# Kernel tuning notes

Hardware: AMD Instinct MI355X
Metric: run time of the kernel (lower is better)

## Reference

```python
import jax, jax.numpy as jnp
import numpy as np

D_MODEL, D_STATE, D_CONV, EXPAND = 768, 16, 4, 2
D_INNER = EXPAND * D_MODEL
DT_RANK = -(-D_MODEL // 16)  # ceil(d_model/16) = 48
LN_EPS = 1e-5


def setup_inputs() -> dict:
    key = jax.random.key(0)
    ks = jax.random.split(key, 12)
    B, L = 8, 1024
    s = 0.02
    x = jax.random.normal(ks[0], (B, L, D_MODEL), jnp.float32)
    ln_g = jnp.ones((D_MODEL,), jnp.float32)
    ln_b = jnp.zeros((D_MODEL,), jnp.float32)
    W_in = jax.random.normal(ks[1], (D_MODEL, 2 * D_INNER), jnp.float32) * s
    conv_w = jax.random.normal(ks[2], (D_INNER, 1, D_CONV), jnp.float32) * s
    conv_b = jnp.zeros((D_INNER,), jnp.float32)
    W_x = jax.random.normal(ks[3], (D_INNER, DT_RANK + 2 * D_STATE), jnp.float32) * s
    W_dt = jax.random.normal(ks[4], (DT_RANK, D_INNER), jnp.float32) * s
    b_dt = jax.random.uniform(ks[5], (D_INNER,), jnp.float32, -4.0, -2.0)  # softplus -> small dt
    # S4D-real init: A_log[d, n] = log(n+1)
    A_log = jnp.log(jnp.tile(jnp.arange(1, D_STATE + 1, dtype=jnp.float32), (D_INNER, 1)))
    Dskip = jnp.ones((D_INNER,), jnp.float32)
    W_out = jax.random.normal(ks[6], (D_INNER, D_MODEL), jnp.float32) * s
    return dict(x=x, ln_g=ln_g, ln_b=ln_b, W_in=W_in, conv_w=conv_w, conv_b=conv_b,
                W_x=W_x, W_dt=W_dt, b_dt=b_dt, A_log=A_log, Dskip=Dskip, W_out=W_out)


def _mamba_mixer(x, ln_g, ln_b, W_in, conv_w, conv_b, W_x, W_dt, b_dt, A_log, Dskip, W_out):
    B, L, _ = x.shape
    d_inner, _, d_conv = conv_w.shape
    d_state = A_log.shape[1]

    # LayerNorm
    mu = x.mean(-1, keepdims=True)
    var = ((x - mu) ** 2).mean(-1, keepdims=True)
    xn = (x - mu) * jax.lax.rsqrt(var + LN_EPS) * ln_g + ln_b

    # Input projection -> (x_part, z gate)
    xz = xn @ W_in                      # (B, L, 2*d_inner)
    xp, z = jnp.split(xz, 2, axis=-1)

    # Causal depthwise conv1d over time
    xc = jax.lax.conv_general_dilated(
        xp.transpose(0, 2, 1), conv_w,
        window_strides=(1,), padding=[(d_conv - 1, 0)],
        dimension_numbers=("NCH", "OIH", "NCH"), feature_group_count=d_inner)
    xc = jax.nn.silu(xc + conv_b[None, :, None]).transpose(0, 2, 1)  # (B, L, d_inner)

    # Selective parameters
    x_dbl = xc @ W_x                    # (B, L, dt_rank + 2*d_state)
    dt, Bm, Cm = jnp.split(x_dbl, [DT_RANK, DT_RANK + d_state], axis=-1)
    dt = jax.nn.softplus(dt @ W_dt + b_dt)   # (B, L, d_inner)
    A = -jnp.exp(A_log)                      # (d_inner, d_state)

    # Selective (S6) scan over time, carrying state h: (B, d_inner, d_state)
    def step(h, inp):
        x_t, dt_t, B_t, C_t = inp            # (B,d_in), (B,d_in), (B,d_state), (B,d_state)
        dA = jnp.exp(dt_t[:, :, None] * A)   # (B, d_inner, d_state)
        h = dA * h + dt_t[:, :, None] * B_t[:, None, :] * x_t[:, :, None]
        y = jnp.einsum('bds,bs->bd', h, C_t)
        return h, y

    h0 = jnp.zeros((B, d_inner, d_state), x.dtype)
    xs = (xc.transpose(1, 0, 2), dt.transpose(1, 0, 2),
          Bm.transpose(1, 0, 2), Cm.transpose(1, 0, 2))
    _, ys = jax.lax.scan(step, h0, xs)       # ys: (L, B, d_inner)
    y = ys.transpose(1, 0, 2) + xc * Dskip

    # Gate, output projection, residual (dropout is identity in eval mode)
    y = y * jax.nn.silu(z)
    return y @ W_out + x


def reference(x, ln_g, ln_b, W_in, conv_w, conv_b, W_x, W_dt, b_dt, A_log, Dskip, W_out):
    return _mamba_mixer(x, ln_g, ln_b, W_in, conv_w, conv_b, W_x, W_dt, b_dt, A_log, Dskip, W_out)
```

## Files before the change

### kernel.cpp

```cpp
#include <hip/hip_runtime.h>

typedef unsigned short u16;
typedef unsigned int u32;
typedef u16 u16x4 __attribute__((ext_vector_type(4)));
typedef u16 u16x8 __attribute__((ext_vector_type(8)));
typedef __bf16 bf16x8 __attribute__((ext_vector_type(8)));
typedef float f32x4 __attribute__((ext_vector_type(4)));

#define DEV static __device__ __forceinline__
#define AS1 __attribute__((address_space(1)))
#define AS3 __attribute__((address_space(3)))

DEV float bf2f(u16 u) {
  union { u32 i; float f; } c; c.i = ((u32)u) << 16; return c.f;
}
DEV u16 f2bf(float f) {
  union { float f; u32 i; } c; c.f = f;
  u32 x = c.i;
  return (u16)((x + 0x7fffu + ((x >> 16) & 1u)) >> 16);
}

DEV void pow_tree(float e1, float* f) {
  f[1] = e1;        f[2] = e1 * e1;   f[3] = f[1] * f[2]; f[4] = f[2] * f[2];
  f[5] = f[1] * f[4]; f[6] = f[2] * f[4]; f[7] = f[3] * f[4]; f[8] = f[4] * f[4];
  f[9] = f[1] * f[8]; f[10] = f[2] * f[8]; f[11] = f[3] * f[8]; f[12] = f[4] * f[8];
  f[13] = f[5] * f[8]; f[14] = f[6] * f[8]; f[15] = f[7] * f[8]; f[16] = f[8] * f[8];
}

__global__ __launch_bounds__(256) void k_ln(const float* __restrict__ x, const float* __restrict__ g,
                                            const float* __restrict__ b, u16* __restrict__ xn) {
  int row = blockIdx.x, t = threadIdx.x;
  const float* xr = x + (size_t)row * 768;
  float v0 = xr[t], v1 = xr[t + 256], v2 = xr[t + 512];
  float s = v0 + v1 + v2, s2 = v0 * v0 + v1 * v1 + v2 * v2;
#pragma unroll
  for (int o = 32; o; o >>= 1) { s += __shfl_xor(s, o, 64); s2 += __shfl_xor(s2, o, 64); }
  __shared__ float ps[4], ps2[4];
  int wv = t >> 6;
  if ((t & 63) == 0) { ps[wv] = s; ps2[wv] = s2; }
  __syncthreads();
  s = ps[0] + ps[1] + ps[2] + ps[3];
  s2 = ps2[0] + ps2[1] + ps2[2] + ps2[3];
  float mu = s * (1.f / 768.f);
  float var = s2 * (1.f / 768.f) - mu * mu;
  float rs = rsqrtf(var + 1e-5f);
  u16* o = xn + (size_t)row * 768;
  o[t]       = f2bf((v0 - mu) * rs * g[t]       + b[t]);
  o[t + 256] = f2bf((v1 - mu) * rs * g[t + 256] + b[t + 256]);
  o[t + 512] = f2bf((v2 - mu) * rs * g[t + 512] + b[t + 512]);
}

__global__ __launch_bounds__(256) void k_prep(const float* __restrict__ Win, const float* __restrict__ Wout,
                                              const float* __restrict__ Wx,
                                              u16* __restrict__ Wt_in, u16* __restrict__ Wt_out,
                                              u16* __restrict__ Wxt) {
  int bid = blockIdx.x, tid = threadIdx.x;
  if (bid < 3456) {
    const float* in; u16* out; int R, C, bx, by;
    if (bid < 2304) { in = Win;  out = Wt_in;  R = 768;  C = 3072; bx = bid % 96; by = bid / 96; }
    else { int b2 = bid - 2304; in = Wout; out = Wt_out; R = 1536; C = 768;  bx = b2 % 24; by = b2 / 24; }
    __shared__ u16 tile[32][33];
    int tx = tid & 31, ty = tid >> 5;
    int x = bx * 32 + tx, y0 = by * 32;
#pragma unroll
    for (int j = 0; j < 32; j += 8)
      tile[ty + j][tx] = f2bf(in[(size_t)(y0 + ty + j) * C + x]);
    __syncthreads();
    int ox = y0 + tx, oy0 = bx * 32;
#pragma unroll
    for (int j = 0; j < 32; j += 8)
      out[(size_t)(oy0 + ty + j) * R + ox] = tile[tx][ty + j];
  } else {
    int idx = (bid - 3456) * 256 + tid;
    int c = idx / 1536, r = idx % 1536;
    Wxt[idx] = (c < 80) ? f2bf(Wx[(size_t)r * 80 + c]) : (u16)0;
  }
}

__global__ __launch_bounds__(256) void k_wdt_prep(const float* __restrict__ Wdt, u16* __restrict__ Wdtt) {
  int idx = blockIdx.x * 256 + threadIdx.x;
  int n = idx >> 6, k = idx & 63;
  Wdtt[idx] = (k < 48) ? f2bf(Wdt[(size_t)k * 1536 + n]) : (u16)0;
}

template <bool OUTF32, int ACT, int TM, bool SPLITK>
__global__ __launch_bounds__(256) void k_gemm(const u16* __restrict__ A, const u16* __restrict__ Bt,
                                              void* __restrict__ Cout, void* __restrict__ C2,
                                              const float* __restrict__ resid, int N, int K, int splitN,
                                              int lda, int ldb, const float* __restrict__ bias) {
  __shared__ u16 As[2][TM * 64];
  __shared__ u16 Bs[2][128 * 64];
  constexpr int MI = TM / 32;
  int tid = threadIdx.x;
  int wave = tid >> 6, lane = tid & 63;
  int l15 = lane & 15, l4 = lane >> 4;
  int m0 = blockIdx.y * TM, n0 = blockIdx.x * 128;
  int wm = (wave >> 1) * (TM / 2), wn = (wave & 1) * 64;
  int rs = tid >> 3, ss = tid & 7;
  int kOff = SPLITK ? blockIdx.z * K : 0;
  const u16* gA = A  + (size_t)(m0 + rs) * lda + kOff + (size_t)(ss ^ (rs & 7)) * 8;
  const u16* gB = Bt + (size_t)(n0 + rs) * ldb + kOff + (size_t)(ss ^ (rs & 7)) * 8;
  int aOff[MI][2], bOff[4][2];
#pragma unroll
  for (int i = 0; i < MI; ++i) {
    int row = wm + i * 16 + l15;
#pragma unroll
    for (int h = 0; h < 2; ++h) aOff[i][h] = row * 64 + ((h * 4 + l4) ^ (row & 7)) * 8;
  }
#pragma unroll
  for (int j = 0; j < 4; ++j) {
    int row = wn + j * 16 + l15;
#pragma unroll
    for (int h = 0; h < 2; ++h) bOff[j][h] = row * 64 + ((h * 4 + l4) ^ (row & 7)) * 8;
  }
  auto stage = [&](int kt, int buf) {
    char* dA = (char*)(&As[buf][0]) + wave * 1024;
    char* dB = (char*)(&Bs[buf][0]) + wave * 1024;
    int k0 = kt * 64;
#pragma unroll
    for (int j = 0; j < MI; ++j)
      __builtin_amdgcn_global_load_lds((const AS1 void*)(gA + k0 + (size_t)j * 32 * lda),
                                       (AS3 void*)(dA + j * 4096), 16, 0, 0);
#pragma unroll
    for (int j = 0; j < 4; ++j)
      __builtin_amdgcn_global_load_lds((const AS1 void*)(gB + k0 + (size_t)j * 32 * ldb),
                                       (AS3 void*)(dB + j * 4096), 16, 0, 0);
  };
  f32x4 acc[MI][4] = {};
  int nt = K >> 6;
  stage(0, 0);
  int cur = 0;
  for (int t = 0; t < nt; ++t) {
    if (t + 1 < nt) stage(t + 1, cur ^ 1);
    __builtin_amdgcn_sched_barrier(0);
    if (t + 1 < nt) {
      if constexpr (TM == 128) asm volatile("s_waitcnt vmcnt(8)" ::: "memory");
      else                     asm volatile("s_waitcnt vmcnt(6)" ::: "memory");
    } else {
      asm volatile("s_waitcnt vmcnt(0)" ::: "memory");
    }
    __builtin_amdgcn_s_barrier();
    __builtin_amdgcn_sched_barrier(0);
    const u16* ab = &As[cur][0];
    const u16* bb = &Bs[cur][0];
    union FragU { u16x8 q; bf16x8 v; } af[MI][2], bfr[4][2];
#pragma unroll
    for (int i = 0; i < MI; ++i) {
      af[i][0].q = *(const u16x8*)(ab + aOff[i][0]);
      af[i][1].q = *(const u16x8*)(ab + aOff[i][1]);
    }
#pragma unroll
    for (int j = 0; j < 4; ++j) {
      bfr[j][0].q = *(const u16x8*)(bb + bOff[j][0]);
      bfr[j][1].q = *(const u16x8*)(bb + bOff[j][1]);
    }
    __builtin_amdgcn_s_setprio(1);
#pragma unroll
    for (int h = 0; h < 2; ++h)
#pragma unroll
      for (int i = 0; i < MI; ++i)
#pragma unroll
        for (int j = 0; j < 4; ++j)
          acc[i][j] = __builtin_amdgcn_mfma_f32_16x16x32_bf16(af[i][h].v, bfr[j][h].v, acc[i][j], 0, 0, 0);
    __builtin_amdgcn_s_setprio(0);
    __builtin_amdgcn_sched_barrier(0);
    __builtin_amdgcn_s_barrier();
    cur ^= 1;
  }
  bool hi = n0 >= splitN;
  int strideOut = hi ? (N - splitN) : splitN;
  int nBase = (hi ? (n0 - splitN) : n0) + wn;
  void* base = hi ? C2 : Cout;
  size_t partOff = SPLITK ? (size_t)blockIdx.z * (size_t)(gridDim.y * TM) * (size_t)strideOut : 0;
#pragma unroll
  for (int i = 0; i < MI; ++i) {
#pragma unroll
    for (int r = 0; r < 4; ++r) {
      int row = m0 + wm + i * 16 + l4 * 4 + r;
      const float* rrow = resid ? (resid + (size_t)row * strideOut + nBase) : nullptr;
#pragma unroll
      for (int j = 0; j < 4; ++j) {
        float v = acc[i][j][r];
        int col = j * 16 + l15;
        if (rrow) v += rrow[col];
        if (ACT == 1) {
          v += bias[nBase + col];
          v = (v > 20.f) ? v : __logf(1.f + __expf(v));
        }
        if (OUTF32)
          ((float*)base)[partOff + (size_t)row * strideOut + nBase + col] = v;
        else
          ((u16*)base)[(size_t)row * strideOut + nBase + col] = f2bf(v);
      }
    }
  }
}

__global__ __launch_bounds__(256) void k_xd_red(const float* __restrict__ part, u16* __restrict__ xd) {
  int i = (blockIdx.x * 256 + threadIdx.x) * 4;
  f32x4 s = *(const f32x4*)(part + i);
#pragma unroll
  for (int q = 1; q < 4; ++q) {
    f32x4 p = *(const f32x4*)(part + (size_t)q * 1048576 + i);
    s[0] += p[0]; s[1] += p[1]; s[2] += p[2]; s[3] += p[3];
  }
  u16x4 o = { f2bf(s[0]), f2bf(s[1]), f2bf(s[2]), f2bf(s[3]) };
  *(u16x4*)(xd + i) = o;
}

__global__ __launch_bounds__(256) void k_conv(const u16* __restrict__ xp, const float* __restrict__ cw,
                                              const float* __restrict__ cb, u16* __restrict__ xc) {
  int idx = blockIdx.x * 256 + threadIdx.x;
  int d8 = idx % 192;
  int blq = idx / 192;
  int lq = blq & 255;
  int b = blq >> 8;
  int l0 = lq * 4;
  int d0 = d8 * 8;

  f32x4 w[8];
#pragma unroll
  for (int e = 0; e < 8; ++e) w[e] = *(const f32x4*)(cw + (d0 + e) * 4);
  f32x4 bi0 = *(const f32x4*)(cb + d0);
  f32x4 bi1 = *(const f32x4*)(cb + d0 + 4);

  const u16* xb = xp + ((size_t)b * 1024) * 1536 + d0;
  u16x8 xrow[7];
#pragma unroll
  for (int j = 0; j < 7; ++j) {
    int l = l0 - 3 + j;
    if (l >= 0) xrow[j] = *(const u16x8*)(xb + (size_t)l * 1536);
    else { u16x8 zz = {}; xrow[j] = zz; }
  }

  u16* ob = xc + ((size_t)b * 1024 + l0) * 1536 + d0;
#pragma unroll
  for (int t = 0; t < 4; ++t) {
    u16x8 o;
#pragma unroll
    for (int e = 0; e < 8; ++e) {
      float acc = (e < 4) ? bi0[e] : bi1[e - 4];
#pragma unroll
      for (int j = 0; j < 4; ++j)
        acc = fmaf(bf2f(xrow[t + j][e]), w[e][j], acc);
      o[e] = f2bf(acc / (1.f + __expf(-acc)));
    }
    *(u16x8*)(ob + (size_t)t * 1536) = o;
  }
}

__global__ __launch_bounds__(256) void k_scanA(const u16* __restrict__ dt, const u16* __restrict__ xc,
                                               const u16* __restrict__ xd,
                                               float* __restrict__ hp, float* __restrict__ sdtg) {
  int d = blockIdx.x * 256 + threadIdx.x;
  int c = blockIdx.y, b = blockIdx.z;
  float h[16] = {};
  float sdt = 0.f;
  size_t t0 = (size_t)b * 1024 + c * 32;
  const u16* dtp = dt + t0 * 1536 + d;
  const u16* xcp = xc + t0 * 1536 + d;
  const u16* xdp = xd + t0 * 128;
  for (int l = 0; l < 32; ++l) {
    float dtv = bf2f(dtp[(size_t)l * 1536]);
    float xv  = bf2f(xcp[(size_t)l * 1536]);
    u16x8 b0 = *(const u16x8*)(xdp + l * 128 + 48);
    u16x8 b1 = *(const u16x8*)(xdp + l * 128 + 56);
    float dx = dtv * xv;
    sdt += dtv;
    float f[17];
    pow_tree(__expf(-dtv), f);
#pragma unroll
    for (int n = 0; n < 16; ++n) {
      float Bv = bf2f(n < 8 ? b0[n] : b1[n - 8]);
      h[n] = fmaf(f[n + 1], h[n], dx * Bv);
    }
  }
  size_t s = (((size_t)(b * 32 + c) * 1536) + d) * 16;
#pragma unroll
  for (int q = 0; q < 4; ++q) {
    f32x4 hv = { h[q * 4], h[q * 4 + 1], h[q * 4 + 2], h[q * 4 + 3] };
    *(f32x4*)(hp + s + q * 4) = hv;
  }
  sdtg[(size_t)(b * 32 + c) * 1536 + d] = sdt;
}

__global__ __launch_bounds__(256) void k_scanB(float* __restrict__ hp, const float* __restrict__ sdtg,
                                               const float* __restrict__ Alog) {
  int dn = blockIdx.x * 256 + threadIdx.x;
  int b = blockIdx.y;
  int d = dn >> 4;
  float An = -__expf(Alog[dn]);
  float h = 0.f;
#pragma unroll 4
  for (int c = 0; c < 32; ++c) {
    size_t s = ((size_t)(b * 32 + c)) * 24576 + dn;
    float p = __expf(An * sdtg[(size_t)(b * 32 + c) * 1536 + d]);
    float v = hp[s];
    hp[s] = h;
    h = fmaf(p, h, v);
  }
}

__global__ __launch_bounds__(256) void k_scanC(u16* xcY, const u16* __restrict__ dt,
                                               const u16* __restrict__ xd, const u16* __restrict__ z,
                                               const float* __restrict__ Dsk,
                                               const float* __restrict__ hp) {
  int d = blockIdx.x * 256 + threadIdx.x;
  int c = blockIdx.y, b = blockIdx.z;
  float h[16];
  size_t s = (((size_t)(b * 32 + c) * 1536) + d) * 16;
#pragma unroll
  for (int q = 0; q < 4; ++q) {
    f32x4 hv = *(const f32x4*)(hp + s + q * 4);
    h[q * 4] = hv[0]; h[q * 4 + 1] = hv[1]; h[q * 4 + 2] = hv[2]; h[q * 4 + 3] = hv[3];
  }
  float Dv = Dsk[d];
  size_t t0 = (size_t)b * 1024 + c * 32;
  const u16* dtp = dt + t0 * 1536 + d;
  u16* xcp = xcY + t0 * 1536 + d;
  const u16* zp = z + t0 * 1536 + d;
  const u16* xdp = xd + t0 * 128;
  for (int l = 0; l < 32; ++l) {
    float dtv = bf2f(dtp[(size_t)l * 1536]);
    float xv  = bf2f(xcp[(size_t)l * 1536]);
    float zv  = bf2f(zp[(size_t)l * 1536]);
    u16x8 b0 = *(const u16x8*)(xdp + l * 128 + 48);
    u16x8 b1 = *(const u16x8*)(xdp + l * 128 + 56);
    u16x8 c0 = *(const u16x8*)(xdp + l * 128 + 64);
    u16x8 c1 = *(const u16x8*)(xdp + l * 128 + 72);
    float dx = dtv * xv;
    float f[17];
    pow_tree(__expf(-dtv), f);
    float y0 = 0.f, y1 = 0.f, y2 = 0.f, y3 = 0.f;
#pragma unroll
    for (int n = 0; n < 16; ++n) {
      float Bv = bf2f(n < 8 ? b0[n] : b1[n - 8]);
      float Cv = bf2f(n < 8 ? c0[n] : c1[n - 8]);
      h[n] = fmaf(f[n + 1], h[n], dx * Bv);
      float hc = h[n] * Cv;
      if ((n & 3) == 0) y0 += hc; else if ((n & 3) == 1) y1 += hc;
      else if ((n & 3) == 2) y2 += hc; else y3 += hc;
    }
    float y = (y0 + y1) + (y2 + y3);
    float gate = zv / (1.f + __expf(-zv));
    xcp[(size_t)l * 1536] = f2bf((y + xv * Dv) * gate);
  }
}

extern "C" void kernel_launch(void* const* d_in, const int* in_sizes, int n_in,
                              void* d_out, int out_size, void* d_ws, size_t ws_size,
                              hipStream_t stream) {
  const float* x      = (const float*)d_in[0];
  const float* ln_g   = (const float*)d_in[1];
  const float* ln_b   = (const float*)d_in[2];
  const float* W_in   = (const float*)d_in[3];
  const float* conv_w = (const float*)d_in[4];
  const float* conv_b = (const float*)d_in[5];
  const float* W_x    = (const float*)d_in[6];
  const float* W_dt   = (const float*)d_in[7];
  const float* b_dt   = (const float*)d_in[8];
  const float* A_log  = (const float*)d_in[9];
  const float* Dskip  = (const float*)d_in[10];
  const float* W_out  = (const float*)d_in[11];

  char* ws = (char*)d_ws;
  u16* xn     = (u16*)(ws);
  float* sdtg = (float*)(ws);
  u16* Wt_in  = (u16*)(ws + 12582912);
  u16* Wdtt   = (u16*)(ws + 12582912);
  u16* Wt_out = (u16*)(ws + 17301504);
  u16* Wxt    = (u16*)(ws + 19660800);
  u16* xp     = (u16*)(ws + 20054016);
  float* hp   = (float*)(ws + 20054016);
  u16* z      = (u16*)(ws + 45219840);
  u16* xc     = (u16*)(ws + 70385664);
  u16* xd     = (u16*)(ws + 95551488);
  u16* dt     = (u16*)(ws + 97648640);
  float* xdP  = (float*)(ws + 97648640);

  k_prep<<<4224, 256, 0, stream>>>(W_in, W_out, W_x, Wt_in, Wt_out, Wxt);
  k_ln<<<8192, 256, 0, stream>>>(x, ln_g, ln_b, xn);
  k_gemm<false, 0, 128, false><<<dim3(24, 64), 256, 0, stream>>>(xn, Wt_in, xp, z, nullptr, 3072, 768, 1536, 768, 768, nullptr);
  k_conv<<<1536, 256, 0, stream>>>(xp, conv_w, conv_b, xc);
  k_wdt_prep<<<384, 256, 0, stream>>>(W_dt, Wdtt);
  k_gemm<true, 0, 64, true><<<dim3(1, 128, 4), 256, 0, stream>>>(xc, Wxt, xdP, nullptr, nullptr, 128, 384, 128, 1536, 1536, nullptr);
  k_xd_red<<<1024, 256, 0, stream>>>(xdP, xd);
  k_gemm<false, 1, 128, false><<<dim3(12, 64), 256, 0, stream>>>(xd, Wdtt, dt, nullptr, nullptr, 1536, 64, 1536, 128, 64, b_dt);
  k_scanA<<<dim3(6, 32, 8), 256, 0, stream>>>(dt, xc, xd, hp, sdtg);
  k_scanB<<<dim3(96, 8), 256, 0, stream>>>(hp, sdtg, A_log);
  k_scanC<<<dim3(6, 32, 8), 256, 0, stream>>>(xc, dt, xd, z, Dskip, hp);
  k_gemm<true, 0, 64, false><<<dim3(6, 128), 256, 0, stream>>>(xc, Wt_out, d_out, nullptr, x, 768, 1536, 768, 1536, 1536, nullptr);
}
```

Measured before the change: 230.2 us.

## Fuse prep kernels, halve GEMM K-tile, and add XCD-aware block remap

Merges the weight-transpose prep and LayerNorm into one launch, and folds the W_dt transpose into the x_dbl split-K reduction kernel, removing two kernel launches. The GEMM K-tile drops from 64 to 32, which halves LDS use and drops the XOR swizzle in favour of a plain row layout. Non-split-K GEMMs also gain a block-id remap that spreads consecutive tiles across the 8 XCDs. The unswizzled 64-byte LDS rows may cause bank conflicts, and the smaller K step doubles the loop iterations and barriers.

```diff
diff --git a/kernel.cpp b/kernel.cpp
--- a/kernel.cpp
+++ b/kernel.cpp
@@ -27,44 +27,42 @@
   f[13] = f[5] * f[8]; f[14] = f[6] * f[8]; f[15] = f[7] * f[8]; f[16] = f[8] * f[8];
 }
 
-__global__ __launch_bounds__(256) void k_ln(const float* __restrict__ x, const float* __restrict__ g,
-                                            const float* __restrict__ b, u16* __restrict__ xn) {
-  int row = blockIdx.x, t = threadIdx.x;
-  const float* xr = x + (size_t)row * 768;
-  float v0 = xr[t], v1 = xr[t + 256], v2 = xr[t + 512];
-  float s = v0 + v1 + v2, s2 = v0 * v0 + v1 * v1 + v2 * v2;
-#pragma unroll
-  for (int o = 32; o; o >>= 1) { s += __shfl_xor(s, o, 64); s2 += __shfl_xor(s2, o, 64); }
+__global__ __launch_bounds__(256) void k_prep_ln(const float* __restrict__ Win, const float* __restrict__ Wout,
+                                                 const float* __restrict__ Wx, const float* __restrict__ x,
+                                                 const float* __restrict__ g, const float* __restrict__ bb,
+                                                 u16* __restrict__ Wt_in, u16* __restrict__ Wt_out,
+                                                 u16* __restrict__ Wxt, u16* __restrict__ xn) {
+  int bid = blockIdx.x, tid = threadIdx.x;
+  __shared__ u16 tile[32][33];
   __shared__ float ps[4], ps2[4];
-  int wv = t >> 6;
-  if ((t & 63) == 0) { ps[wv] = s; ps2[wv] = s2; }
-  __syncthreads();
-  s = ps[0] + ps[1] + ps[2] + ps[3];
-  s2 = ps2[0] + ps2[1] + ps2[2] + ps2[3];
-  float mu = s * (1.f / 768.f);
-  float var = s2 * (1.f / 768.f) - mu * mu;
-  float rs = rsqrtf(var + 1e-5f);
-  u16* o = xn + (size_t)row * 768;
-  o[t]       = f2bf((v0 - mu) * rs * g[t]       + b[t]);
-  o[t + 256] = f2bf((v1 - mu) * rs * g[t + 256] + b[t + 256]);
-  o[t + 512] = f2bf((v2 - mu) * rs * g[t + 512] + b[t + 512]);
-}
-
-__global__ __launch_bounds__(256) void k_prep(const float* __restrict__ Win, const float* __restrict__ Wout,
-                                              const float* __restrict__ Wx,
-                                              u16* __restrict__ Wt_in, u16* __restrict__ Wt_out,
-                                              u16* __restrict__ Wxt) {
-  int bid = blockIdx.x, tid = threadIdx.x;
-  if (bid < 3456) {
+  if (bid >= 4224) {
+    int row = bid - 4224;
+    const float* xr = x + (size_t)row * 768;
+    float v0 = xr[tid], v1 = xr[tid + 256], v2 = xr[tid + 512];
+    float s = v0 + v1 + v2, s2 = v0 * v0 + v1 * v1 + v2 * v2;
+#pragma unroll
+    for (int o = 32; o; o >>= 1) { s += __shfl_xor(s, o, 64); s2 += __shfl_xor(s2, o, 64); }
+    int wv = tid >> 6;
+    if ((tid & 63) == 0) { ps[wv] = s; ps2[wv] = s2; }
+    __syncthreads();
+    s = ps[0] + ps[1] + ps[2] + ps[3];
+    s2 = ps2[0] + ps2[1] + ps2[2] + ps2[3];
+    float mu = s * (1.f / 768.f);
+    float var = s2 * (1.f / 768.f) - mu * mu;
+    float rs = rsqrtf(var + 1e-5f);
+    u16* o = xn + (size_t)row * 768;
+    o[tid]       = f2bf((v0 - mu) * rs * g[tid]       + bb[tid]);
+    o[tid + 256] = f2bf((v1 - mu) * rs * g[tid + 256] + bb[tid + 256]);
+    o[tid + 512] = f2bf((v2 - mu) * rs * g[tid + 512] + bb[tid + 512]);
+  } else if (bid < 3456) {
     const float* in; u16* out; int R, C, bx, by;
     if (bid < 2304) { in = Win;  out = Wt_in;  R = 768;  C = 3072; bx = bid % 96; by = bid / 96; }
     else { int b2 = bid - 2304; in = Wout; out = Wt_out; R = 1536; C = 768;  bx = b2 % 24; by = b2 / 24; }
-    __shared__ u16 tile[32][33];
     int tx = tid & 31, ty = tid >> 5;
-    int x = bx * 32 + tx, y0 = by * 32;
+    int xx = bx * 32 + tx, y0 = by * 32;
 #pragma unroll
     for (int j = 0; j < 32; j += 8)
-      tile[ty + j][tx] = f2bf(in[(size_t)(y0 + ty + j) * C + x]);
+      tile[ty + j][tx] = f2bf(in[(size_t)(y0 + ty + j) * C + xx]);
     __syncthreads();
     int ox = y0 + tx, oy0 = bx * 32;
 #pragma unroll
@@ -77,65 +75,62 @@
   }
 }
 
-__global__ __launch_bounds__(256) void k_wdt_prep(const float* __restrict__ Wdt, u16* __restrict__ Wdtt) {
-  int idx = blockIdx.x * 256 + threadIdx.x;
-  int n = idx >> 6, k = idx & 63;
-  Wdtt[idx] = (k < 48) ? f2bf(Wdt[(size_t)k * 1536 + n]) : (u16)0;
-}
-
 template <bool OUTF32, int ACT, int TM, bool SPLITK>
 __global__ __launch_bounds__(256) void k_gemm(const u16* __restrict__ A, const u16* __restrict__ Bt,
                                               void* __restrict__ Cout, void* __restrict__ C2,
                                               const float* __restrict__ resid, int N, int K, int splitN,
                                               int lda, int ldb, const float* __restrict__ bias) {
-  __shared__ u16 As[2][TM * 64];
-  __shared__ u16 Bs[2][128 * 64];
+  __shared__ u16 As[2][TM * 32];
+  __shared__ u16 Bs[2][128 * 32];
   constexpr int MI = TM / 32;
   int tid = threadIdx.x;
   int wave = tid >> 6, lane = tid & 63;
   int l15 = lane & 15, l4 = lane >> 4;
-  int m0 = blockIdx.y * TM, n0 = blockIdx.x * 128;
+  int bx = blockIdx.x, by = blockIdx.y;
+  if (!SPLITK) {
+    int gx = gridDim.x;
+    int nwg = gx * gridDim.y;
+    if ((nwg & 7) == 0) {
+      int bid = by * gx + bx;
+      int bid2 = (bid & 7) * (nwg >> 3) + (bid >> 3);
+      bx = bid2 % gx;
+      by = bid2 / gx;
+    }
+  }
+  int m0 = by * TM, n0 = bx * 128;
   int wm = (wave >> 1) * (TM / 2), wn = (wave & 1) * 64;
-  int rs = tid >> 3, ss = tid & 7;
+  int rs = tid >> 2, ss = tid & 3;
   int kOff = SPLITK ? blockIdx.z * K : 0;
-  const u16* gA = A  + (size_t)(m0 + rs) * lda + kOff + (size_t)(ss ^ (rs & 7)) * 8;
-  const u16* gB = Bt + (size_t)(n0 + rs) * ldb + kOff + (size_t)(ss ^ (rs & 7)) * 8;
-  int aOff[MI][2], bOff[4][2];
-#pragma unroll
-  for (int i = 0; i < MI; ++i) {
-    int row = wm + i * 16 + l15;
-#pragma unroll
-    for (int h = 0; h < 2; ++h) aOff[i][h] = row * 64 + ((h * 4 + l4) ^ (row & 7)) * 8;
-  }
-#pragma unroll
-  for (int j = 0; j < 4; ++j) {
-    int row = wn + j * 16 + l15;
-#pragma unroll
-    for (int h = 0; h < 2; ++h) bOff[j][h] = row * 64 + ((h * 4 + l4) ^ (row & 7)) * 8;
-  }
+  const u16* gA = A  + (size_t)(m0 + rs) * lda + kOff + (size_t)ss * 8;
+  const u16* gB = Bt + (size_t)(n0 + rs) * ldb + kOff + (size_t)ss * 8;
+  int aOff[MI], bOff[4];
+#pragma unroll
+  for (int i = 0; i < MI; ++i) aOff[i] = (wm + i * 16 + l15) * 32 + l4 * 8;
+#pragma unroll
+  for (int j = 0; j < 4; ++j)  bOff[j] = (wn + j * 16 + l15) * 32 + l4 * 8;
   auto stage = [&](int kt, int buf) {
     char* dA = (char*)(&As[buf][0]) + wave * 1024;
     char* dB = (char*)(&Bs[buf][0]) + wave * 1024;
-    int k0 = kt * 64;
-#pragma unroll
-    for (int j = 0; j < MI; ++j)
-      __builtin_amdgcn_global_load_lds((const AS1 void*)(gA + k0 + (size_t)j * 32 * lda),
+    int k0 = kt * 32;
+#pragma unroll
+    for (int j = 0; j < TM / 64; ++j)
+      __builtin_amdgcn_global_load_lds((const AS1 void*)(gA + k0 + (size_t)j * 64 * lda),
                                        (AS3 void*)(dA + j * 4096), 16, 0, 0);
 #pragma unroll
-    for (int j = 0; j < 4; ++j)
-      __builtin_amdgcn_global_load_lds((const AS1 void*)(gB + k0 + (size_t)j * 32 * ldb),
+    for (int j = 0; j < 2; ++j)
+      __builtin_amdgcn_global_load_lds((const AS1 void*)(gB + k0 + (size_t)j * 64 * ldb),
                                        (AS3 void*)(dB + j * 4096), 16, 0, 0);
   };
   f32x4 acc[MI][4] = {};
-  int nt = K >> 6;
+  int nt = K >> 5;
   stage(0, 0);
   int cur = 0;
   for (int t = 0; t < nt; ++t) {
     if (t + 1 < nt) stage(t + 1, cur ^ 1);
     __builtin_amdgcn_sched_barrier(0);
     if (t + 1 < nt) {
-      if constexpr (TM == 128) asm volatile("s_waitcnt vmcnt(8)" ::: "memory");
-      else                     asm volatile("s_waitcnt vmcnt(6)" ::: "memory");
+      if constexpr (TM == 128) asm volatile("s_waitcnt vmcnt(4)" ::: "memory");
+      else                     asm volatile("s_waitcnt vmcnt(3)" ::: "memory");
     } else {
       asm volatile("s_waitcnt vmcnt(0)" ::: "memory");
     }
@@ -143,25 +138,17 @@
     __builtin_amdgcn_sched_barrier(0);
     const u16* ab = &As[cur][0];
     const u16* bb = &Bs[cur][0];
-    union FragU { u16x8 q; bf16x8 v; } af[MI][2], bfr[4][2];
-#pragma unroll
-    for (int i = 0; i < MI; ++i) {
-      af[i][0].q = *(const u16x8*)(ab + aOff[i][0]);
-      af[i][1].q = *(const u16x8*)(ab + aOff[i][1]);
-    }
-#pragma unroll
-    for (int j = 0; j < 4; ++j) {
-      bfr[j][0].q = *(const u16x8*)(bb + bOff[j][0]);
-      bfr[j][1].q = *(const u16x8*)(bb + bOff[j][1]);
-    }
+    union FragU { u16x8 q; bf16x8 v; } af[MI], bfr[4];
+#pragma unroll
+    for (int i = 0; i < MI; ++i) af[i].q = *(const u16x8*)(ab + aOff[i]);
+#pragma unroll
+    for (int j = 0; j < 4; ++j)  bfr[j].q = *(const u16x8*)(bb + bOff[j]);
     __builtin_amdgcn_s_setprio(1);
 #pragma unroll
-    for (int h = 0; h < 2; ++h)
-#pragma unroll
-      for (int i = 0; i < MI; ++i)
-#pragma unroll
-        for (int j = 0; j < 4; ++j)
-          acc[i][j] = __builtin_amdgcn_mfma_f32_16x16x32_bf16(af[i][h].v, bfr[j][h].v, acc[i][j], 0, 0, 0);
+    for (int i = 0; i < MI; ++i)
+#pragma unroll
+      for (int j = 0; j < 4; ++j)
+        acc[i][j] = __builtin_amdgcn_mfma_f32_16x16x32_bf16(af[i].v, bfr[j].v, acc[i][j], 0, 0, 0);
     __builtin_amdgcn_s_setprio(0);
     __builtin_amdgcn_sched_barrier(0);
     __builtin_amdgcn_s_barrier();
@@ -196,16 +183,24 @@
   }
 }
 
-__global__ __launch_bounds__(256) void k_xd_red(const float* __restrict__ part, u16* __restrict__ xd) {
-  int i = (blockIdx.x * 256 + threadIdx.x) * 4;
-  f32x4 s = *(const f32x4*)(part + i);
-#pragma unroll
-  for (int q = 1; q < 4; ++q) {
-    f32x4 p = *(const f32x4*)(part + (size_t)q * 1048576 + i);
-    s[0] += p[0]; s[1] += p[1]; s[2] += p[2]; s[3] += p[3];
-  }
-  u16x4 o = { f2bf(s[0]), f2bf(s[1]), f2bf(s[2]), f2bf(s[3]) };
-  *(u16x4*)(xd + i) = o;
+__global__ __launch_bounds__(256) void k_xd_red_wdt(const float* __restrict__ part, u16* __restrict__ xd,
+                                                    const float* __restrict__ Wdt, u16* __restrict__ Wdtt) {
+  int bid = blockIdx.x, tid = threadIdx.x;
+  if (bid < 1024) {
+    int i = (bid * 256 + tid) * 4;
+    f32x4 s = *(const f32x4*)(part + i);
+#pragma unroll
+    for (int q = 1; q < 4; ++q) {
+      f32x4 p = *(const f32x4*)(part + (size_t)q * 1048576 + i);
+      s[0] += p[0]; s[1] += p[1]; s[2] += p[2]; s[3] += p[3];
+    }
+    u16x4 o = { f2bf(s[0]), f2bf(s[1]), f2bf(s[2]), f2bf(s[3]) };
+    *(u16x4*)(xd + i) = o;
+  } else {
+    int idx = (bid - 1024) * 256 + tid;
+    int n = idx >> 6, k = idx & 63;
+    Wdtt[idx] = (k < 48) ? f2bf(Wdt[(size_t)k * 1536 + n]) : (u16)0;
+  }
 }
 
 __global__ __launch_bounds__(256) void k_conv(const u16* __restrict__ xp, const float* __restrict__ cw,
@@ -378,13 +373,11 @@
   u16* dt     = (u16*)(ws + 97648640);
   float* xdP  = (float*)(ws + 97648640);
 
-  k_prep<<<4224, 256, 0, stream>>>(W_in, W_out, W_x, Wt_in, Wt_out, Wxt);
-  k_ln<<<8192, 256, 0, stream>>>(x, ln_g, ln_b, xn);
+  k_prep_ln<<<12416, 256, 0, stream>>>(W_in, W_out, W_x, x, ln_g, ln_b, Wt_in, Wt_out, Wxt, xn);
   k_gemm<false, 0, 128, false><<<dim3(24, 64), 256, 0, stream>>>(xn, Wt_in, xp, z, nullptr, 3072, 768, 1536, 768, 768, nullptr);
   k_conv<<<1536, 256, 0, stream>>>(xp, conv_w, conv_b, xc);
-  k_wdt_prep<<<384, 256, 0, stream>>>(W_dt, Wdtt);
   k_gemm<true, 0, 64, true><<<dim3(1, 128, 4), 256, 0, stream>>>(xc, Wxt, xdP, nullptr, nullptr, 128, 384, 128, 1536, 1536, nullptr);
-  k_xd_red<<<1024, 256, 0, stream>>>(xdP, xd);
+  k_xd_red_wdt<<<1408, 256, 0, stream>>>(xdP, xd, W_dt, Wdtt);
   k_gemm<false, 1, 128, false><<<dim3(12, 64), 256, 0, stream>>>(xd, Wdtt, dt, nullptr, nullptr, 1536, 64, 1536, 128, 64, b_dt);
   k_scanA<<<dim3(6, 32, 8), 256, 0, stream>>>(dt, xc, xd, hp, sdtg);
   k_scanB<<<dim3(96, 8), 256, 0, stream>>>(hp, sdtg, A_log);
```

Measured after the change: 232.1 us. Within noise of the previous version (+0.8%).
